# Kernel tuning notes

Hardware: AMD Instinct MI355X
Metric: run time of the kernel (lower is better)

Reference implementation:

```python
import jax, jax.numpy as jnp
import numpy as np

DIM = 1024
HEAD_DIM = 64
NUM_HEADS = DIM // HEAD_DIM
SCALE = HEAD_DIM ** -0.5
B, N, M = 2, 1024, 2048


def setup_inputs() -> dict:
    key = jax.random.key(0)
    ks = jax.random.split(key, 7)
    x = jax.random.normal(ks[0], (B, N, DIM), dtype=jnp.float32)
    context = jax.random.normal(ks[1], (B, M, DIM), dtype=jnp.float32)
    # query row has at least one valid key (avoids all -inf softmax rows).
    mask = jax.random.bernoulli(ks[2], 0.9, (B, N, M))
    mask = mask.at[:, :, 0].set(True)
    # Linear params (torch nn.Linear convention: y = x @ W.T + b)
    sq = (1.0 / DIM) ** 0.5
    Wq = jax.random.uniform(ks[3], (DIM, DIM), minval=-sq, maxval=sq, dtype=jnp.float32)
    Wkv = jax.random.uniform(ks[4], (2 * DIM, DIM), minval=-sq, maxval=sq, dtype=jnp.float32)
    b_kv = jax.random.uniform(ks[5], (2 * DIM,), minval=-sq, maxval=sq, dtype=jnp.float32)
    Wo = jax.random.uniform(ks[6], (DIM, DIM), minval=-sq, maxval=sq, dtype=jnp.float32)
    return {"x": x, "context": context, "mask": mask,
            "Wq": Wq, "Wkv": Wkv, "b_kv": b_kv, "Wo": Wo}


def reference(x, context, mask, Wq, Wkv, b_kv, Wo):
    b, n, c = x.shape
    m = context.shape[1]
    h, d = NUM_HEADS, HEAD_DIM
    # Q projection (no bias): [b, n, h, d] -> bhnd
    q = (x @ Wq.T).reshape(b, n, h, d).transpose(0, 2, 1, 3)
    # KV projection (with bias): [b, m, 2, h, d]
    kv = (context @ Wkv.T + b_kv).reshape(b, m, 2, h, d)
    k = kv[:, :, 0].transpose(0, 2, 1, 3)  # bhmd
    v = kv[:, :, 1].transpose(0, 2, 1, 3)  # bhmd
    # scores: bhnm, scale applied after matmul as in the original
    attn = jnp.einsum('bhnd,bhmd->bhnm', q, k) * SCALE
    attn = jnp.where(mask[:, None, :, :], attn, -jnp.inf)
    attn = jax.nn.softmax(attn, axis=-1)
    out = jnp.einsum('bhnm,bhmd->bhnd', attn, v)
    out = out.transpose(0, 2, 1, 3).reshape(b, n, h * d)
    return out @ Wo.T
```

## Files before the change

### kernel.cpp

```cpp
#include <hip/hip_runtime.h>


typedef __attribute__((ext_vector_type(8))) short short8;
typedef __attribute__((ext_vector_type(4))) short short4v;
typedef __attribute__((ext_vector_type(4))) float f32x4;
typedef __attribute__((ext_vector_type(4))) int int4v;

#define SCL2E 0.18033688011112042592f

__device__ __forceinline__ float bf2f(short s) {
  unsigned u = ((unsigned)(unsigned short)s) << 16;
  return __uint_as_float(u);
}
__device__ __forceinline__ short f2bf(float f) {
  unsigned u = __float_as_uint(f);
  u += 0x7fffu + ((u >> 16) & 1u);
  return (short)(u >> 16);
}
__device__ __forceinline__ int cvt_pk_bf16(float a, float b) {
  int r;
  asm("v_cvt_pk_bf16_f32 %0, %1, %2" : "=v"(r) : "v"(a), "v"(b));
  return r;
}
__device__ __forceinline__ void gld_lds16(const void* gp, void* lp) {
  __builtin_amdgcn_global_load_lds(
      (const __attribute__((address_space(1))) unsigned int*)gp,
      (__attribute__((address_space(3))) unsigned int*)lp, 16, 0, 0);
}
__device__ __forceinline__ short4v cvt4(float4 v) {
  short4v o;
  o[0] = f2bf(v.x); o[1] = f2bf(v.y); o[2] = f2bf(v.z); o[3] = f2bf(v.w);
  return o;
}
__device__ __forceinline__ size_t off128(int row, int k) {
  return ((size_t)(((row >> 7) * 32 + (k >> 5)) * 8 + ((row >> 4) & 7)) << 9) +
         (((((k >> 3) & 3) * 16 + (row & 15)) << 3) + (k & 7));
}
__device__ __forceinline__ size_t off64(int row, int k) {
  return ((size_t)(((row >> 6) * 32 + (k >> 5)) * 4 + ((row >> 4) & 3)) << 9) +
         (((((k >> 3) & 3) * 16 + (row & 15)) << 3) + (k & 7));
}

__global__ __launch_bounds__(256) void prep(
    const unsigned char* __restrict__ mask, unsigned long long* __restrict__ pm,
    const float* __restrict__ Wq, const float* __restrict__ Wkv,
    const float* __restrict__ Wo, const float* __restrict__ x,
    const float* __restrict__ ctx, short* __restrict__ wqb,
    short* __restrict__ wkvb, short* __restrict__ wob,
    short* __restrict__ xb, short* __restrict__ ctxb) {
  const int row = blockIdx.x;
  const int wave = threadIdx.x >> 6, lane = threadIdx.x & 63;
  const unsigned char p8 = mask[lane * 4 + 1];
  const int p32 = ((const int*)mask)[lane * 2 + 1];
  const int shift =
      (__ballot(p8 != 0) != 0ull) ? 0 : ((__ballot(p32 != 0) != 0ull) ? 2 : 3);
  const size_t mbase = ((size_t)row * 2048) << shift;
#pragma unroll
  for (int j = 0; j < 8; j++) {
    const int c = wave * 512 + j * 64 + lane;
    const unsigned long long bits = __ballot(mask[mbase + ((size_t)c << shift)] != 0);
    if (lane == 0) pm[(size_t)row * 32 + wave * 8 + j] = bits;
  }
  const int gid = blockIdx.x * 256 + threadIdx.x;
  {
    const int e = gid * 4, r = e >> 10, k = e & 1023;
    *(short4v*)(xb + off128(r, k)) = cvt4(((const float4*)x)[gid]);
  }
  {
    int e = gid * 4, r = e >> 10, k = e & 1023;
    *(short4v*)(ctxb + off128(r, k)) = cvt4(((const float4*)ctx)[gid]);
    e = (gid + 524288) * 4; r = e >> 10; k = e & 1023;
    *(short4v*)(ctxb + off128(r, k)) = cvt4(((const float4*)ctx)[gid + 524288]);
  }
  {
    const int e = gid * 4, r = e >> 10, k = e & 1023;
    *(short4v*)(wkvb + off128(r, k)) = cvt4(((const float4*)Wkv)[gid]);
  }
  if (gid < 262144) {
    const int e = gid * 4, r = e >> 10, k = e & 1023;
    *(short4v*)(wqb + off128(r, k)) = cvt4(((const float4*)Wq)[gid]);
    *(short4v*)(wob + off64(r, k)) = cvt4(((const float4*)Wo)[gid]);
  }
}

__global__ __launch_bounds__(256, 2)
void qkv_gemm(const short* __restrict__ xb, const short* __restrict__ ctxb,
              const short* __restrict__ wqb, const short* __restrict__ wkvb,
              const float* __restrict__ bias, short* __restrict__ qws,
              short* __restrict__ kws, short* __restrict__ vtws) {
  __shared__ __align__(16) short ldsA[8 * 512];
  __shared__ __align__(16) short ldsB[8 * 512];
  const int tid = threadIdx.x;
  const int wave = tid >> 6, lane = tid & 63;
  const int l15 = lane & 15, lg = lane >> 4;
  const int bx = blockIdx.x;
  const bool isKV = bx < 512;
  const int rt = isKV ? (bx >> 4) : ((bx - 512) >> 3);
  const int ct = isKV ? (bx & 15) : ((bx - 512) & 7);
  const short* Amat = isKV ? ctxb : xb;
  const short* Bw = isKV ? wkvb : wqb;
  const int wr = wave >> 1, wc = wave & 1;

  f32x4 acc[4][4];
#pragma unroll
  for (int i = 0; i < 4; i++)
#pragma unroll
    for (int j = 0; j < 4; j++) acc[i][j] = (f32x4){0.f, 0.f, 0.f, 0.f};

  const short* ga0 = Amat + (size_t)rt * 131072 + wave * 512 + lane * 8;
  const short* ga1 = ga0 + 2048;
  const short* gb0 = Bw + (size_t)ct * 131072 + wave * 512 + lane * 8;
  const short* gb1 = gb0 + 2048;
  short* la0 = &ldsA[wave * 512];
  short* la1 = &ldsA[(wave + 4) * 512];
  short* lb0 = &ldsB[wave * 512];
  short* lb1 = &ldsB[(wave + 4) * 512];

  for (int k0 = 0; k0 < 1024; k0 += 32) {
    const size_t koff = (size_t)(k0 >> 5) * 4096;
    __syncthreads();
    gld_lds16(ga0 + koff, la0);
    gld_lds16(ga1 + koff, la1);
    gld_lds16(gb0 + koff, lb0);
    gld_lds16(gb1 + koff, lb1);
    __syncthreads();
    short8 af[4], bfr[4];
#pragma unroll
    for (int t = 0; t < 4; t++)
      af[t] = *(const short8*)&ldsA[((wr * 4 + t) * 64 + lane) * 8];
#pragma unroll
    for (int t = 0; t < 4; t++)
      bfr[t] = *(const short8*)&ldsB[((wc * 4 + t) * 64 + lane) * 8];
#pragma unroll
    for (int i = 0; i < 4; i++)
#pragma unroll
      for (int j = 0; j < 4; j++)
        acc[i][j] =
            __builtin_amdgcn_mfma_f32_16x16x32_bf16(af[i], bfr[j], acc[i][j], 0, 0, 0);
  }

#pragma unroll
  for (int i = 0; i < 4; i++)
#pragma unroll
    for (int j = 0; j < 4; j++)
#pragma unroll
      for (int r = 0; r < 4; r++) {
        const int gr = rt * 128 + wr * 64 + i * 16 + lg * 4 + r;
        const int gc = ct * 128 + wc * 64 + j * 16 + l15;
        float v = acc[i][j][r];
        if (isKV) {
          v += bias[gc];
          const int b = gr >> 11, m = gr & 2047;
          const int kv = gc >> 10, hh = (gc >> 6) & 15, d = gc & 63;
          if (kv == 0)
            kws[((((size_t)b * 16 + hh) * 2048 + m) << 6) + d] = f2bf(v);
          else {
            const int mp = (m & ~31) | (((m >> 2) & 3) << 3) |
                           (((m >> 4) & 1) << 2) | (m & 3);
            vtws[(((size_t)b * 16 + hh) * 64 + d) * 2048 + mp] = f2bf(v);
          }
        } else {
          const int b = gr >> 10, n = gr & 1023, hh = gc >> 6, d = gc & 63;
          qws[((((size_t)b * 16 + hh) * 1024 + n) << 6) + d] = f2bf(v * SCL2E);
        }
      }
}

__global__ __launch_bounds__(512, 6)
void attn_split(const short* __restrict__ Qg, const short* __restrict__ Kg,
                const short* __restrict__ Vtg,
                const unsigned int* __restrict__ pm,
                float* __restrict__ opart, float* __restrict__ lpart) {
  __shared__ __align__(16) short ldsK[8192];
  __shared__ __align__(16) short ldsV[8192];
  const int tid = threadIdx.x;
  const int w = tid >> 6, lane = tid & 63;
  const int l15 = lane & 15, lg = lane >> 4;
  const int bx = blockIdx.x;
  const int bhid = bx & 31, qt = (bx >> 5) & 7, half = bx >> 8;
  const int b = bhid >> 4, h = bhid & 15;
  const int n0 = qt * 128, m_base = half * 1024;
  const size_t bh = (size_t)b * 16 + h;
  const short* Qb = Qg + (bh * 1024 + n0) * 64;
  const short* Kb = Kg + (bh << 17);
  const short* Vb = Vtg + (bh << 17);
  const unsigned int* pmw =
      pm + ((size_t)(b * 1024 + n0 + w * 16 + l15) << 6) + (m_base >> 5);

#pragma unroll
  for (int ii = 0; ii < 2; ii++)
    gld_lds16(Qb + (size_t)(w * 16 + l15) * 64 + ii * 32 + lg * 8,
              &ldsK[(w * 2 + ii) * 512]);
  __syncthreads();
  short8 qf[2];
#pragma unroll
  for (int ks = 0; ks < 2; ks++)
    qf[ks] = *(const short8*)&ldsK[((w * 2 + ks) * 64 + lane) * 8];

  short8 onesf;
#pragma unroll
  for (int i = 0; i < 8; i++) onesf[i] = (short)0x3F80;

  f32x4 o[4], lacc;
#pragma unroll
  for (int ct = 0; ct < 4; ct++) o[ct] = (f32x4){0.f, 0.f, 0.f, 0.f};
  lacc = (f32x4){0.f, 0.f, 0.f, 0.f};
  const int sb = lg * 4;

  for (int c = 0; c < 8; c++) {
    const int m0 = m_base + c * 128;
    const uint4 mk = *(const uint4*)(pmw + c * 4);
    __syncthreads();
#pragma unroll
    for (int ii = 0; ii < 2; ii++) {
      const int f = w * 2 + ii;
      const int t = f >> 1, ks = f & 1;
      gld_lds16(Kb + (size_t)(m0 + t * 16 + l15) * 64 + ks * 32 + lg * 8,
                &ldsK[f * 512]);
      const int vt = f >> 2, vk = f & 3;
      gld_lds16(Vb + (size_t)(vt * 16 + l15) * 2048 + (m0 + vk * 32 + lg * 8),
                &ldsV[f * 512]);
    }
    __syncthreads();

    int4v pw4[4];
#pragma unroll
    for (int h2 = 0; h2 < 2; h2++) {
      f32x4 s[4];
#pragma unroll
      for (int t2 = 0; t2 < 4; t2++) s[t2] = (f32x4){0.f, 0.f, 0.f, 0.f};
#pragma unroll
      for (int t2 = 0; t2 < 4; t2++) {
        const int t = h2 * 4 + t2;
#pragma unroll
        for (int ks = 0; ks < 2; ks++) {
          const short8 kf = *(const short8*)&ldsK[((t * 2 + ks) * 64 + lane) * 8];
          s[t2] = __builtin_amdgcn_mfma_f32_16x16x32_bf16(kf, qf[ks], s[t2], 0, 0, 0);
        }
      }
#pragma unroll
      for (int t2 = 0; t2 < 4; t2++) {
        const int t = h2 * 4 + t2;
        const unsigned int mw = ((t >> 1) == 0) ? mk.x
                              : ((t >> 1) == 1) ? mk.y
                              : ((t >> 1) == 2) ? mk.z : mk.w;
        float p[4];
#pragma unroll
        for (int r = 0; r < 4; r++) {
          const bool att = (mw >> (((t & 1) << 4) + sb + r)) & 1;
          p[r] = exp2f(att ? s[t2][r] : -1e30f);
        }
        pw4[t >> 1][(t & 1) * 2] = cvt_pk_bf16(p[0], p[1]);
        pw4[t >> 1][(t & 1) * 2 + 1] = cvt_pk_bf16(p[2], p[3]);
      }
    }

#pragma unroll
    for (int ks2 = 0; ks2 < 4; ks2++) {
      const short8 pf = __builtin_bit_cast(short8, pw4[ks2]);
#pragma unroll
      for (int ct = 0; ct < 4; ct++) {
        const short8 vf = *(const short8*)&ldsV[((ct * 4 + ks2) * 64 + lane) * 8];
        o[ct] = __builtin_amdgcn_mfma_f32_16x16x32_bf16(pf, vf, o[ct], 0, 0, 0);
      }
      lacc = __builtin_amdgcn_mfma_f32_16x16x32_bf16(pf, onesf, lacc, 0, 0, 0);
    }
  }

#pragma unroll
  for (int ct = 0; ct < 4; ct++)
#pragma unroll
    for (int r = 0; r < 4; r++) {
      const int n = n0 + w * 16 + lg * 4 + r;
      opart[((size_t)half << 21) + (((size_t)b * 1024 + n) << 10) + h * 64 +
            ct * 16 + l15] = o[ct][r];
    }
  if (l15 == 0) {
#pragma unroll
    for (int r = 0; r < 4; r++) {
      const int n = n0 + w * 16 + lg * 4 + r;
      lpart[((size_t)half << 15) + bh * 1024 + n] = lacc[r];
    }
  }
}

__global__ __launch_bounds__(256) void combine(
    const float* __restrict__ opart, const float* __restrict__ lpart,
    short* __restrict__ aoT) {
  const int gid = blockIdx.x * 256 + threadIdx.x;
  const size_t base = (size_t)gid * 4;
  const int row = (int)(base >> 10), col = (int)(base & 1023);
  const int b = row >> 10, n = row & 1023, h = col >> 6;
  const float4 o1 = *(const float4*)(opart + base);
  const float4 o2 = *(const float4*)(opart + (1u << 21) + base);
  const float l1 = lpart[(size_t)(b * 16 + h) * 1024 + n];
  const float l2 = lpart[(1u << 15) + (size_t)(b * 16 + h) * 1024 + n];
  const float inv = 1.f / fmaxf(l1 + l2, 1e-30f);
  short4v o;
  o[0] = f2bf((o1.x + o2.x) * inv); o[1] = f2bf((o1.y + o2.y) * inv);
  o[2] = f2bf((o1.z + o2.z) * inv); o[3] = f2bf((o1.w + o2.w) * inv);
  *(short4v*)(aoT + off64(row, col)) = o;
}

__global__ __launch_bounds__(256, 2)
void o_gemm(const short* __restrict__ aoT, const short* __restrict__ wobT,
            float* __restrict__ Of) {
  __shared__ __align__(16) short ldsA[4 * 512];
  __shared__ __align__(16) short ldsB[4 * 512];
  const int tid = threadIdx.x;
  const int w = tid >> 6, lane = tid & 63;
  const int l15 = lane & 15, lg = lane >> 4;
  const int bx = blockIdx.x;
  const int rt = bx >> 4, ct = bx & 15;

  f32x4 acc[4];
#pragma unroll
  for (int j = 0; j < 4; j++) acc[j] = (f32x4){0.f, 0.f, 0.f, 0.f};

  const short* ga = aoT + (size_t)rt * 65536 + w * 512 + lane * 8;
  const short* gb = wobT + (size_t)ct * 65536 + w * 512 + lane * 8;
  short* la = &ldsA[w * 512];
  short* lb = &ldsB[w * 512];

  for (int k0 = 0; k0 < 1024; k0 += 32) {
    const size_t koff = (size_t)(k0 >> 5) * 2048;
    __syncthreads();
    gld_lds16(ga + koff, la);
    gld_lds16(gb + koff, lb);
    __syncthreads();
    const short8 af = *(const short8*)&ldsA[(w * 64 + lane) * 8];
#pragma unroll
    for (int j = 0; j < 4; j++) {
      const short8 bf = *(const short8*)&ldsB[(j * 64 + lane) * 8];
      acc[j] = __builtin_amdgcn_mfma_f32_16x16x32_bf16(af, bf, acc[j], 0, 0, 0);
    }
  }

#pragma unroll
  for (int j = 0; j < 4; j++)
#pragma unroll
    for (int r = 0; r < 4; r++) {
      const int gr = rt * 64 + w * 16 + lg * 4 + r;
      const int gc = ct * 64 + j * 16 + l15;
      Of[(size_t)gr * 1024 + gc] = acc[j][r];
    }
}

extern "C" void kernel_launch(void* const* d_in, const int* in_sizes, int n_in,
                              void* d_out, int out_size, void* d_ws, size_t ws_size,
                              hipStream_t stream) {
  const float* x   = (const float*)d_in[0];
  const float* ctx = (const float*)d_in[1];
  const unsigned char* mask = (const unsigned char*)d_in[2];
  const float* Wq  = (const float*)d_in[3];
  const float* Wkv = (const float*)d_in[4];
  const float* bkv = (const float*)d_in[5];
  const float* Wo  = (const float*)d_in[6];
  float* out = (float*)d_out;

  char* wsb = (char*)d_ws;
  short* qws  = (short*)(wsb);
  short* kws  = (short*)(wsb + (4u << 20));
  short* vtws = (short*)(wsb + (12u << 20));
  short* wqb  = (short*)(wsb + (20u << 20));
  short* wkvb = (short*)(wsb + (22u << 20));
  short* wob  = (short*)(wsb + (26u << 20));
  unsigned long long* pmws = (unsigned long long*)(wsb + (28u << 20));
  float* opart = (float*)(wsb + (29u << 20));
  float* lpart = (float*)(wsb + (45u << 20));
  short* xb   = (short*)(wsb + (29u << 20));
  short* ctxb = (short*)(wsb + (33u << 20));
  short* ao = (short*)(wsb + (20u << 20));

  prep<<<2048, 256, 0, stream>>>(mask, pmws, Wq, Wkv, Wo, x, ctx,
                                 wqb, wkvb, wob, xb, ctxb);
  qkv_gemm<<<640, 256, 0, stream>>>(xb, ctxb, wqb, wkvb, bkv, qws, kws, vtws);
  attn_split<<<512, 512, 0, stream>>>(qws, kws, vtws, (const unsigned int*)pmws,
                                      opart, lpart);
  combine<<<2048, 256, 0, stream>>>(opart, lpart, ao);
  o_gemm<<<512, 256, 0, stream>>>(ao, wob, out);
}
```

Before: 232.9 us.

## Double-buffer LDS tiles in qkv, attention and output GEMM kernels

Converts the three main kernels from a load-sync-compute loop to a two-stage ping-pong pipeline. The next K/V or A/B tile is issued with global_load_lds into the alternate LDS buffer while the current one is consumed, using a custom waitcnt-plus-barrier sync. This aims to hide global memory latency behind MFMA work. LDS use doubles, and the attention kernel's occupancy hint drops from 6 to 4 blocks per CU to fit.

```diff
diff --git a/kernel.cpp b/kernel.cpp
--- a/kernel.cpp
+++ b/kernel.cpp
@@ -26,6 +26,12 @@
   __builtin_amdgcn_global_load_lds(
       (const __attribute__((address_space(1))) unsigned int*)gp,
       (__attribute__((address_space(3))) unsigned int*)lp, 16, 0, 0);
+}
+__device__ __forceinline__ void pipesync() {
+  asm volatile("s_waitcnt vmcnt(0) lgkmcnt(0)" ::: "memory");
+  __builtin_amdgcn_sched_barrier(0);
+  __builtin_amdgcn_s_barrier();
+  __builtin_amdgcn_sched_barrier(0);
 }
 __device__ __forceinline__ short4v cvt4(float4 v) {
   short4v o;
@@ -88,8 +94,8 @@
               const short* __restrict__ wqb, const short* __restrict__ wkvb,
               const float* __restrict__ bias, short* __restrict__ qws,
               short* __restrict__ kws, short* __restrict__ vtws) {
-  __shared__ __align__(16) short ldsA[8 * 512];
-  __shared__ __align__(16) short ldsB[8 * 512];
+  __shared__ __align__(16) short ldsA[2][4096];
+  __shared__ __align__(16) short ldsB[2][4096];
   const int tid = threadIdx.x;
   const int wave = tid >> 6, lane = tid & 63;
   const int l15 = lane & 15, lg = lane >> 4;
@@ -111,32 +117,39 @@
   const short* ga1 = ga0 + 2048;
   const short* gb0 = Bw + (size_t)ct * 131072 + wave * 512 + lane * 8;
   const short* gb1 = gb0 + 2048;
-  short* la0 = &ldsA[wave * 512];
-  short* la1 = &ldsA[(wave + 4) * 512];
-  short* lb0 = &ldsB[wave * 512];
-  short* lb1 = &ldsB[(wave + 4) * 512];
-
-  for (int k0 = 0; k0 < 1024; k0 += 32) {
-    const size_t koff = (size_t)(k0 >> 5) * 4096;
-    __syncthreads();
-    gld_lds16(ga0 + koff, la0);
-    gld_lds16(ga1 + koff, la1);
-    gld_lds16(gb0 + koff, lb0);
-    gld_lds16(gb1 + koff, lb1);
-    __syncthreads();
+
+  auto stage = [&](int kk, short* dA, short* dB) {
+    const size_t koff = (size_t)kk * 4096;
+    gld_lds16(ga0 + koff, dA + wave * 512);
+    gld_lds16(ga1 + koff, dA + (wave + 4) * 512);
+    gld_lds16(gb0 + koff, dB + wave * 512);
+    gld_lds16(gb1 + koff, dB + (wave + 4) * 512);
+  };
+  auto compute = [&](const short* sA, const short* sB) {
     short8 af[4], bfr[4];
 #pragma unroll
     for (int t = 0; t < 4; t++)
-      af[t] = *(const short8*)&ldsA[((wr * 4 + t) * 64 + lane) * 8];
+      af[t] = *(const short8*)&sA[((wr * 4 + t) * 64 + lane) * 8];
 #pragma unroll
     for (int t = 0; t < 4; t++)
-      bfr[t] = *(const short8*)&ldsB[((wc * 4 + t) * 64 + lane) * 8];
+      bfr[t] = *(const short8*)&sB[((wc * 4 + t) * 64 + lane) * 8];
 #pragma unroll
     for (int i = 0; i < 4; i++)
 #pragma unroll
       for (int j = 0; j < 4; j++)
         acc[i][j] =
             __builtin_amdgcn_mfma_f32_16x16x32_bf16(af[i], bfr[j], acc[i][j], 0, 0, 0);
+  };
+
+  stage(0, ldsA[0], ldsB[0]);
+  pipesync();
+  for (int kk = 0; kk < 32; kk += 2) {
+    if (kk + 1 < 32) stage(kk + 1, ldsA[1], ldsB[1]);
+    compute(ldsA[0], ldsB[0]);
+    pipesync();
+    if (kk + 2 < 32) stage(kk + 2, ldsA[0], ldsB[0]);
+    compute(ldsA[1], ldsB[1]);
+    pipesync();
   }
 
 #pragma unroll
@@ -166,13 +179,13 @@
       }
 }
 
-__global__ __launch_bounds__(512, 6)
+__global__ __launch_bounds__(512, 4)
 void attn_split(const short* __restrict__ Qg, const short* __restrict__ Kg,
                 const short* __restrict__ Vtg,
                 const unsigned int* __restrict__ pm,
                 float* __restrict__ opart, float* __restrict__ lpart) {
-  __shared__ __align__(16) short ldsK[8192];
-  __shared__ __align__(16) short ldsV[8192];
+  __shared__ __align__(16) short ldsK[2][8192];
+  __shared__ __align__(16) short ldsV[2][8192];
   const int tid = threadIdx.x;
   const int w = tid >> 6, lane = tid & 63;
   const int l15 = lane & 15, lg = lane >> 4;
@@ -187,42 +200,47 @@
   const unsigned int* pmw =
       pm + ((size_t)(b * 1024 + n0 + w * 16 + l15) << 6) + (m_base >> 5);
 
-#pragma unroll
-  for (int ii = 0; ii < 2; ii++)
-    gld_lds16(Qb + (size_t)(w * 16 + l15) * 64 + ii * 32 + lg * 8,
-              &ldsK[(w * 2 + ii) * 512]);
-  __syncthreads();
-  short8 qf[2];
-#pragma unroll
-  for (int ks = 0; ks < 2; ks++)
-    qf[ks] = *(const short8*)&ldsK[((w * 2 + ks) * 64 + lane) * 8];
-
-  short8 onesf;
-#pragma unroll
-  for (int i = 0; i < 8; i++) onesf[i] = (short)0x3F80;
-
-  f32x4 o[4], lacc;
-#pragma unroll
-  for (int ct = 0; ct < 4; ct++) o[ct] = (f32x4){0.f, 0.f, 0.f, 0.f};
-  lacc = (f32x4){0.f, 0.f, 0.f, 0.f};
-  const int sb = lg * 4;
-
-  for (int c = 0; c < 8; c++) {
+  auto stageKV = [&](int c, short* dK, short* dV) {
     const int m0 = m_base + c * 128;
-    const uint4 mk = *(const uint4*)(pmw + c * 4);
-    __syncthreads();
 #pragma unroll
     for (int ii = 0; ii < 2; ii++) {
       const int f = w * 2 + ii;
       const int t = f >> 1, ks = f & 1;
       gld_lds16(Kb + (size_t)(m0 + t * 16 + l15) * 64 + ks * 32 + lg * 8,
-                &ldsK[f * 512]);
+                dK + f * 512);
       const int vt = f >> 2, vk = f & 3;
       gld_lds16(Vb + (size_t)(vt * 16 + l15) * 2048 + (m0 + vk * 32 + lg * 8),
-                &ldsV[f * 512]);
-    }
-    __syncthreads();
-
+                dV + f * 512);
+    }
+  };
+
+#pragma unroll
+  for (int ii = 0; ii < 2; ii++)
+    gld_lds16(Qb + (size_t)(w * 16 + l15) * 64 + ii * 32 + lg * 8,
+              &ldsK[0][(w * 2 + ii) * 512]);
+  stageKV(0, ldsK[1], ldsV[1]);
+  pipesync();
+  short8 qf[2];
+#pragma unroll
+  for (int ks = 0; ks < 2; ks++)
+    qf[ks] = *(const short8*)&ldsK[0][((w * 2 + ks) * 64 + lane) * 8];
+  asm volatile("s_waitcnt lgkmcnt(0)" ::: "memory");
+  __builtin_amdgcn_sched_barrier(0);
+  __builtin_amdgcn_s_barrier();
+  __builtin_amdgcn_sched_barrier(0);
+
+  short8 onesf;
+#pragma unroll
+  for (int i = 0; i < 8; i++) onesf[i] = (short)0x3F80;
+
+  f32x4 o[4], lacc;
+#pragma unroll
+  for (int ct = 0; ct < 4; ct++) o[ct] = (f32x4){0.f, 0.f, 0.f, 0.f};
+  lacc = (f32x4){0.f, 0.f, 0.f, 0.f};
+  const int sb = lg * 4;
+
+  auto computeC = [&](int c, const short* sK, const short* sV) {
+    const uint4 mk = *(const uint4*)(pmw + c * 4);
     int4v pw4[4];
 #pragma unroll
     for (int h2 = 0; h2 < 2; h2++) {
@@ -234,7 +252,7 @@
         const int t = h2 * 4 + t2;
 #pragma unroll
         for (int ks = 0; ks < 2; ks++) {
-          const short8 kf = *(const short8*)&ldsK[((t * 2 + ks) * 64 + lane) * 8];
+          const short8 kf = *(const short8*)&sK[((t * 2 + ks) * 64 + lane) * 8];
           s[t2] = __builtin_amdgcn_mfma_f32_16x16x32_bf16(kf, qf[ks], s[t2], 0, 0, 0);
         }
       }
@@ -254,17 +272,25 @@
         pw4[t >> 1][(t & 1) * 2 + 1] = cvt_pk_bf16(p[2], p[3]);
       }
     }
-
 #pragma unroll
     for (int ks2 = 0; ks2 < 4; ks2++) {
       const short8 pf = __builtin_bit_cast(short8, pw4[ks2]);
 #pragma unroll
       for (int ct = 0; ct < 4; ct++) {
-        const short8 vf = *(const short8*)&ldsV[((ct * 4 + ks2) * 64 + lane) * 8];
+        const short8 vf = *(const short8*)&sV[((ct * 4 + ks2) * 64 + lane) * 8];
         o[ct] = __builtin_amdgcn_mfma_f32_16x16x32_bf16(pf, vf, o[ct], 0, 0, 0);
       }
       lacc = __builtin_amdgcn_mfma_f32_16x16x32_bf16(pf, onesf, lacc, 0, 0, 0);
     }
+  };
+
+  for (int c = 0; c < 8; c += 2) {
+    if (c + 1 < 8) stageKV(c + 1, ldsK[0], ldsV[0]);
+    computeC(c, ldsK[1], ldsV[1]);
+    pipesync();
+    if (c + 2 < 8) stageKV(c + 2, ldsK[1], ldsV[1]);
+    computeC(c + 1, ldsK[0], ldsV[0]);
+    pipesync();
   }
 
 #pragma unroll
@@ -305,8 +331,8 @@
 __global__ __launch_bounds__(256, 2)
 void o_gemm(const short* __restrict__ aoT, const short* __restrict__ wobT,
             float* __restrict__ Of) {
-  __shared__ __align__(16) short ldsA[4 * 512];
-  __shared__ __align__(16) short ldsB[4 * 512];
+  __shared__ __align__(16) short ldsA[2][2048];
+  __shared__ __align__(16) short ldsB[2][2048];
   const int tid = threadIdx.x;
   const int w = tid >> 6, lane = tid & 63;
   const int l15 = lane & 15, lg = lane >> 4;
@@ -319,21 +345,30 @@
 
   const short* ga = aoT + (size_t)rt * 65536 + w * 512 + lane * 8;
   const short* gb = wobT + (size_t)ct * 65536 + w * 512 + lane * 8;
-  short* la = &ldsA[w * 512];
-  short* lb = &ldsB[w * 512];
-
-  for (int k0 = 0; k0 < 1024; k0 += 32) {
-    const size_t koff = (size_t)(k0 >> 5) * 2048;
-    __syncthreads();
-    gld_lds16(ga + koff, la);
-    gld_lds16(gb + koff, lb);
-    __syncthreads();
-    const short8 af = *(const short8*)&ldsA[(w * 64 + lane) * 8];
+
+  auto stage = [&](int kk, short* dA, short* dB) {
+    const size_t koff = (size_t)kk * 2048;
+    gld_lds16(ga + koff, dA + w * 512);
+    gld_lds16(gb + koff, dB + w * 512);
+  };
+  auto compute = [&](const short* sA, const short* sB) {
+    const short8 af = *(const short8*)&sA[(w * 64 + lane) * 8];
 #pragma unroll
     for (int j = 0; j < 4; j++) {
-      const short8 bf = *(const short8*)&ldsB[(j * 64 + lane) * 8];
+      const short8 bf = *(const short8*)&sB[(j * 64 + lane) * 8];
       acc[j] = __builtin_amdgcn_mfma_f32_16x16x32_bf16(af, bf, acc[j], 0, 0, 0);
     }
+  };
+
+  stage(0, ldsA[0], ldsB[0]);
+  pipesync();
+  for (int kk = 0; kk < 32; kk += 2) {
+    if (kk + 1 < 32) stage(kk + 1, ldsA[1], ldsB[1]);
+    compute(ldsA[0], ldsB[0]);
+    pipesync();
+    if (kk + 2 < 32) stage(kk + 2, ldsA[0], ldsB[0]);
+    compute(ldsA[1], ldsB[1]);
+    pipesync();
   }
 
 #pragma unroll
```

Result: no change. 235.6 us (+1.2%).
